# Performance work log

Measured on AMD Instinct MI355X. Metric: run time of the kernel, lower is better.

## Reference

```python
import jax, jax.numpy as jnp
import numpy as np

B, N, D, E, ET, L = 2, 50000, 64, 400000, 200000, 6
R_STRUCT = 4
EPS = 1e-5


def _ln(x, g, b):
    m = jnp.mean(x, axis=-1, keepdims=True)
    v = jnp.mean((x - m) ** 2, axis=-1, keepdims=True)
    return (x - m) * jax.lax.rsqrt(v + EPS) * g + b


def _nbf(boundary, src, dst, rel_e_fn, W, b, g, beta):
    # One RelNBFNet / TextRelNBFNet stack of GeneralizedRelationalConv layers:
    #   distmult message, sum aggregation with boundary self-loop message,
    #   linear([x, agg]) -> layernorm -> relu, short_cut residual.
    # boundary: [B, N, D]
    x = boundary
    for i in range(W.shape[0]):
        msg = x[:, src, :] * rel_e_fn(i)                    # [B, E, D]
        agg = jnp.zeros_like(x).at[:, dst, :].add(msg) + boundary
        h = jnp.concatenate([x, agg], axis=-1) @ W[i] + b[i]
        h = jax.nn.relu(_ln(h, g[i], beta[i]))
        x = h + x                                           # short_cut
    return x


def setup_inputs() -> dict:
    key = jax.random.key(0)
    ks = jax.random.split(key, 16)
    s = 0.05
    return {
        "rel_text_init": jax.random.normal(ks[0], (N, D), jnp.float32),
        "struct_rel": jax.random.normal(ks[1], (L, R_STRUCT, D), jnp.float32) * s,
        "struct_W": jax.random.normal(ks[2], (L, 2 * D, D), jnp.float32) * s,
        "struct_b": jnp.zeros((L, D), jnp.float32),
        "struct_g": jnp.ones((L, D), jnp.float32),
        "struct_beta": jnp.zeros((L, D), jnp.float32),
        "text_rel": jax.random.normal(ks[3], (L, 1, D), jnp.float32) * s,
        "text_W": jax.random.normal(ks[4], (L, 2 * D, D), jnp.float32) * s,
        "text_b": jnp.zeros((L, D), jnp.float32),
        "text_g": jnp.ones((L, D), jnp.float32),
        "text_beta": jnp.zeros((L, D), jnp.float32),
        "fuse_W1": jax.random.normal(ks[5], (2 * D, D), jnp.float32) * s,
        "fuse_b1": jnp.zeros((D,), jnp.float32),
        "fuse_W2": jax.random.normal(ks[6], (D, D), jnp.float32) * s,
        "fuse_b2": jnp.zeros((D,), jnp.float32),
        "h_index": jax.random.randint(ks[7], (B,), 0, N),
        "edge_index": jax.random.randint(ks[8], (2, E), 0, N),
        "edge_type": jax.random.randint(ks[9], (E,), 0, R_STRUCT),
        "text_edge_index": jax.random.randint(ks[10], (2, ET), 0, N),
    }


def reference(rel_text_init, struct_rel, struct_W, struct_b, struct_g, struct_beta,
              text_rel, text_W, text_b, text_g, text_beta,
              fuse_W1, fuse_b1, fuse_W2, fuse_b2,
              h_index, edge_index, edge_type, text_edge_index):
    # struct branch: boundary = indicator at query relation node
    boundary_s = jnp.zeros((B, N, D), rel_text_init.dtype).at[jnp.arange(B), h_index].add(1.0)
    h = _nbf(boundary_s, edge_index[0], edge_index[1],
             lambda i: struct_rel[i][edge_type],
             struct_W, struct_b, struct_g, struct_beta)
    # text branch: boundary = text-derived init features, single relation type
    boundary_t = jnp.broadcast_to(rel_text_init[None], (B, N, D))
    z = _nbf(boundary_t, text_edge_index[0], text_edge_index[1],
             lambda i: text_rel[i, 0][None, None, :],
             text_W, text_b, text_g, text_beta)
    # mlp fusion (alpha = 1.0)
    f = jax.nn.relu(jnp.concatenate([h, z], axis=-1) @ fuse_W1 + fuse_b1)
    return f @ fuse_W2 + fuse_b2
```

## Files before the change

### kernel.cpp

```cpp
#include <hip/hip_runtime.h>


__device__ __forceinline__ float bf2f(unsigned short u) {
    return __uint_as_float(((unsigned)u) << 16);
}
__device__ __forceinline__ unsigned short f2bf(float f) {
    unsigned u = __float_as_uint(f);
    u += 0x7FFF + ((u >> 16) & 1);
    return (unsigned short)(u >> 16);
}
#define PACK2(a, b) ((unsigned)f2bf(a) | ((unsigned)f2bf(b) << 16))

__device__ __forceinline__ float4 lnout(float4 A, float m, float inv,
                                        float4 xv, float4 gg, float4 bb) {
    float4 y;
    y.x = fmaxf((A.x - m) * inv * gg.x + bb.x, 0.f) + xv.x;
    y.y = fmaxf((A.y - m) * inv * gg.y + bb.y, 0.f) + xv.y;
    y.z = fmaxf((A.z - m) * inv * gg.z + bb.z, 0.f) + xv.z;
    y.w = fmaxf((A.w - m) * inv * gg.w + bb.w, 0.f) + xv.w;
    return y;
}

#define FMA4R(v, wbase, R0, R1, R2, R3) do {                                  \
    const float4* _w = (const float4*)(wbase); float4 _t;                     \
    _t=_w[0]; R0.x=fmaf(v,_t.x,R0.x); R0.y=fmaf(v,_t.y,R0.y); R0.z=fmaf(v,_t.z,R0.z); R0.w=fmaf(v,_t.w,R0.w); \
    _t=_w[1]; R1.x=fmaf(v,_t.x,R1.x); R1.y=fmaf(v,_t.y,R1.y); R1.z=fmaf(v,_t.z,R1.z); R1.w=fmaf(v,_t.w,R1.w); \
    _t=_w[2]; R2.x=fmaf(v,_t.x,R2.x); R2.y=fmaf(v,_t.y,R2.y); R2.z=fmaf(v,_t.z,R2.z); R2.w=fmaf(v,_t.w,R2.w); \
    _t=_w[3]; R3.x=fmaf(v,_t.x,R3.x); R3.y=fmaf(v,_t.y,R3.y); R3.z=fmaf(v,_t.z,R3.z); R3.w=fmaf(v,_t.w,R3.w); \
} while (0)

#define FMA4R2(v0, v1, wbase, P0,P1,P2,P3, Q0,Q1,Q2,Q3) do {                  \
    const float4* _w = (const float4*)(wbase); float4 _t;                     \
    _t=_w[0];                                                                 \
    P0.x=fmaf(v0,_t.x,P0.x); P0.y=fmaf(v0,_t.y,P0.y); P0.z=fmaf(v0,_t.z,P0.z); P0.w=fmaf(v0,_t.w,P0.w); \
    Q0.x=fmaf(v1,_t.x,Q0.x); Q0.y=fmaf(v1,_t.y,Q0.y); Q0.z=fmaf(v1,_t.z,Q0.z); Q0.w=fmaf(v1,_t.w,Q0.w); \
    _t=_w[1];                                                                 \
    P1.x=fmaf(v0,_t.x,P1.x); P1.y=fmaf(v0,_t.y,P1.y); P1.z=fmaf(v0,_t.z,P1.z); P1.w=fmaf(v0,_t.w,P1.w); \
    Q1.x=fmaf(v1,_t.x,Q1.x); Q1.y=fmaf(v1,_t.y,Q1.y); Q1.z=fmaf(v1,_t.z,Q1.z); Q1.w=fmaf(v1,_t.w,Q1.w); \
    _t=_w[2];                                                                 \
    P2.x=fmaf(v0,_t.x,P2.x); P2.y=fmaf(v0,_t.y,P2.y); P2.z=fmaf(v0,_t.z,P2.z); P2.w=fmaf(v0,_t.w,P2.w); \
    Q2.x=fmaf(v1,_t.x,Q2.x); Q2.y=fmaf(v1,_t.y,Q2.y); Q2.z=fmaf(v1,_t.z,Q2.z); Q2.w=fmaf(v1,_t.w,Q2.w); \
    _t=_w[3];                                                                 \
    P3.x=fmaf(v0,_t.x,P3.x); P3.y=fmaf(v0,_t.y,P3.y); P3.z=fmaf(v0,_t.z,P3.z); P3.w=fmaf(v0,_t.w,P3.w); \
    Q3.x=fmaf(v1,_t.x,Q3.x); Q3.y=fmaf(v1,_t.y,Q3.y); Q3.z=fmaf(v1,_t.z,Q3.z); Q3.w=fmaf(v1,_t.w,Q3.w); \
} while (0)

#define SUM4(Ai) ((Ai.x + Ai.y) + (Ai.z + Ai.w))
#define VAR4M(Ai, mm, vv) do { float _c;                                      \
    _c = Ai.x - mm; vv = fmaf(_c, _c, vv); _c = Ai.y - mm; vv = fmaf(_c, _c, vv); \
    _c = Ai.z - mm; vv = fmaf(_c, _c, vv); _c = Ai.w - mm; vv = fmaf(_c, _c, vv); \
} while (0)

#define RSEL(ty) (((ty) < 2) ? ((ty) == 0 ? r0 : r1) : ((ty) == 2 ? r2 : r3))

__global__ __launch_bounds__(256) void k_init_onehot(
    float* __restrict__ x, unsigned* __restrict__ xmir,
    const int* __restrict__ h_index, int N, int total, int b2)
{
    int idx = blockIdx.x * 256 + threadIdx.x;
    if (idx >= total) return;
    int row = idx >> 6;
    int b = row / N;
    int n = row - b * N;
    x[idx] = (n == h_index[b]) ? 1.0f : 0.0f;
    if (b2 && idx < N * 64) {
        int nn = idx >> 6;
        unsigned w = ((nn == h_index[0]) ? 0x3F80u : 0u)
                   | (((nn == h_index[1]) ? 0x3F80u : 0u) << 16);
        xmir[idx] = w;
    }
}

__global__ __launch_bounds__(256) void k_cast_init(
    const float* __restrict__ init, float* __restrict__ x,
    unsigned short* __restrict__ xbf, int total)
{
    int idx = blockIdx.x * 256 + threadIdx.x;
    if (idx >= total) return;
    float f = init[idx];
    x[idx] = f;
    xbf[idx] = f2bf(f);
}

__global__ __launch_bounds__(256) void k_hist_all(
    const int* __restrict__ dst_s, const int* __restrict__ dst_t,
    int* __restrict__ cnt_s, int* __restrict__ cnt_t, int E, int ET)
{
    int i = blockIdx.x * 256 + threadIdx.x;
    if (i < E) atomicAdd(&cnt_s[dst_s[i]], 1);
    else if (i < E + ET) atomicAdd(&cnt_t[dst_t[i - E]], 1);
}

__global__ __launch_bounds__(1024) void k_scan_blk2(
    const int* __restrict__ cnt_s, int* __restrict__ off_s, int* __restrict__ bsum_s,
    const int* __restrict__ cnt_t, int* __restrict__ off_t, int* __restrict__ bsum_t,
    int n, int nb)
{
    bool tpath = blockIdx.x >= nb;
    int lb = tpath ? blockIdx.x - nb : blockIdx.x;
    const int* cnt = tpath ? cnt_t : cnt_s;
    int* off = tpath ? off_t : off_s;
    int* bsum = tpath ? bsum_t : bsum_s;

    __shared__ int wsum[16], wpre[16], tot;
    int tid = threadIdx.x, lane = tid & 63, w = tid >> 6;
    int i = lb * 1024 + tid;
    int v = (i < n) ? cnt[i] : 0;
    int s = v;
    #pragma unroll
    for (int d = 1; d < 64; d <<= 1) {
        int t = __shfl_up(s, d);
        if (lane >= d) s += t;
    }
    if (lane == 63) wsum[w] = s;
    __syncthreads();
    if (w == 0 && lane < 16) {
        int ws = wsum[lane];
        int p = ws;
        #pragma unroll
        for (int d = 1; d < 16; d <<= 1) {
            int t = __shfl_up(p, d);
            if (lane >= d) p += t;
        }
        wpre[lane] = p - ws;
        if (lane == 15) tot = p;
    }
    __syncthreads();
    if (i < n) off[i + 1] = wpre[w] + s;
    if (tid == 0) {
        bsum[lb] = tot;
        if (lb == 0) off[0] = 0;
    }
}

__global__ __launch_bounds__(1024) void k_scan_top2(
    int* __restrict__ bsum_s, int* __restrict__ bsum_t, int nb)
{
    int* bsum = (blockIdx.x == 0) ? bsum_s : bsum_t;
    __shared__ int wsum[16], wpre[16];
    int tid = threadIdx.x, lane = tid & 63, w = tid >> 6;
    int v = (tid < nb) ? bsum[tid] : 0;
    int s = v;
    #pragma unroll
    for (int d = 1; d < 64; d <<= 1) {
        int t = __shfl_up(s, d);
        if (lane >= d) s += t;
    }
    if (lane == 63) wsum[w] = s;
    __syncthreads();
    if (w == 0 && lane < 16) {
        int ws = wsum[lane];
        int p = ws;
        #pragma unroll
        for (int d = 1; d < 16; d <<= 1) {
            int t = __shfl_up(p, d);
            if (lane >= d) p += t;
        }
        wpre[lane] = p - ws;
    }
    __syncthreads();
    if (tid < nb) bsum[tid] = wpre[w] + s - v;
}

__global__ __launch_bounds__(1024) void k_scan_add2(
    const int* __restrict__ bsum_s, int* __restrict__ off_s,
    const int* __restrict__ bsum_t, int* __restrict__ off_t, int n, int nb)
{
    bool tpath = blockIdx.x >= nb;
    int lb = tpath ? blockIdx.x - nb : blockIdx.x;
    int i = lb * 1024 + threadIdx.x;
    if (i < n) (tpath ? off_t : off_s)[i + 1] += (tpath ? bsum_t : bsum_s)[lb];
}

__global__ __launch_bounds__(256) void k_fill_all(
    const int* __restrict__ src_s, const int* __restrict__ dst_s,
    const int* __restrict__ etype,
    const int* __restrict__ off_s, int* __restrict__ cnt_s, int* __restrict__ pk_s,
    const int* __restrict__ src_t, const int* __restrict__ dst_t,
    const int* __restrict__ off_t, int* __restrict__ cnt_t, int* __restrict__ pk_t,
    int E, int ET)
{
    int i = blockIdx.x * 256 + threadIdx.x;
    if (i < E) {
        int d = dst_s[i];
        int pos = off_s[d] + atomicSub(&cnt_s[d], 1) - 1;
        pk_s[pos] = src_s[i] | (etype[i] << 27);
    } else if (i < E + ET) {
        int e = i - E;
        int d = dst_t[e];
        int pos = off_t[d] + atomicSub(&cnt_t[d], 1) - 1;
        pk_t[pos] = src_t[e];
    }
}

__global__ __launch_bounds__(256) void k_gather_all(
    const unsigned* __restrict__ xws, float* __restrict__ aggs,
    const int* __restrict__ offs, const int* __restrict__ pks,
    const float* __restrict__ rels,
    const int* __restrict__ hidx,
    const unsigned short* __restrict__ xbt, float* __restrict__ aggt,
    const int* __restrict__ offt, const int* __restrict__ pkt,
    const float* __restrict__ relt,
    const float* __restrict__ init,
    int N, int sblocks, int tblocks)
{
    int tid = threadIdx.x;
    int lane = tid & 63;
    bool isStruct; int lb;
    if (sblocks == tblocks) { isStruct = !(blockIdx.x & 1); lb = blockIdx.x >> 1; }
    else if ((int)blockIdx.x < sblocks) { isStruct = true; lb = blockIdx.x; }
    else { isStruct = false; lb = blockIdx.x - sblocks; }
    int n = (lb * 256 + tid) >> 6;
    if (n >= N) return;

    if (isStruct) {
        float r0 = rels[lane], r1 = rels[64 + lane];
        float r2 = rels[128 + lane], r3 = rels[192 + lane];
        float acc0 = (n == hidx[0]) ? 1.0f : 0.0f;
        float acc1 = (n == hidx[1]) ? 1.0f : 0.0f;
        int p0 = __builtin_amdgcn_readfirstlane(offs[n]);
        int p1 = __builtin_amdgcn_readfirstlane(offs[n + 1]);
        for (int p = p0; p < p1; p += 64) {
            int myPk = (p + lane < p1) ? pks[p + lane] : 0;
            int cnt = min(p1 - p, 64);
            int i = 0;
            for (; i + 8 <= cnt; i += 8) {
                int k0 = __shfl(myPk, i + 0), k1 = __shfl(myPk, i + 1);
                int k2 = __shfl(myPk, i + 2), k3 = __shfl(myPk, i + 3);
                int k4 = __shfl(myPk, i + 4), k5 = __shfl(myPk, i + 5);
                int k6 = __shfl(myPk, i + 6), k7 = __shfl(myPk, i + 7);
                unsigned w0 = xws[(size_t)(k0 & 0x03FFFFFF) * 64 + lane];
                unsigned w1 = xws[(size_t)(k1 & 0x03FFFFFF) * 64 + lane];
                unsigned w2 = xws[(size_t)(k2 & 0x03FFFFFF) * 64 + lane];
                unsigned w3 = xws[(size_t)(k3 & 0x03FFFFFF) * 64 + lane];
                unsigned w4 = xws[(size_t)(k4 & 0x03FFFFFF) * 64 + lane];
                unsigned w5 = xws[(size_t)(k5 & 0x03FFFFFF) * 64 + lane];
                unsigned w6 = xws[(size_t)(k6 & 0x03FFFFFF) * 64 + lane];
                unsigned w7 = xws[(size_t)(k7 & 0x03FFFFFF) * 64 + lane];
                int t0 = k0 >> 27, t1 = k1 >> 27, t2 = k2 >> 27, t3 = k3 >> 27;
                int t4 = k4 >> 27, t5 = k5 >> 27, t6 = k6 >> 27, t7 = k7 >> 27;
                float ra = RSEL(t0), rb = RSEL(t1), rc = RSEL(t2), rd = RSEL(t3);
                float re = RSEL(t4), rf = RSEL(t5), rg = RSEL(t6), rh = RSEL(t7);
                acc0 = fmaf(bf2f((unsigned short)w0), ra, acc0);
                acc1 = fmaf(bf2f((unsigned short)(w0 >> 16)), ra, acc1);
                acc0 = fmaf(bf2f((unsigned short)w1), rb, acc0);
                acc1 = fmaf(bf2f((unsigned short)(w1 >> 16)), rb, acc1);
                acc0 = fmaf(bf2f((unsigned short)w2), rc, acc0);
                acc1 = fmaf(bf2f((unsigned short)(w2 >> 16)), rc, acc1);
                acc0 = fmaf(bf2f((unsigned short)w3), rd, acc0);
                acc1 = fmaf(bf2f((unsigned short)(w3 >> 16)), rd, acc1);
                acc0 = fmaf(bf2f((unsigned short)w4), re, acc0);
                acc1 = fmaf(bf2f((unsigned short)(w4 >> 16)), re, acc1);
                acc0 = fmaf(bf2f((unsigned short)w5), rf, acc0);
                acc1 = fmaf(bf2f((unsigned short)(w5 >> 16)), rf, acc1);
                acc0 = fmaf(bf2f((unsigned short)w6), rg, acc0);
                acc1 = fmaf(bf2f((unsigned short)(w6 >> 16)), rg, acc1);
                acc0 = fmaf(bf2f((unsigned short)w7), rh, acc0);
                acc1 = fmaf(bf2f((unsigned short)(w7 >> 16)), rh, acc1);
            }
            for (; i < cnt; ++i) {
                int pk = __shfl(myPk, i);
                int s = pk & 0x03FFFFFF, ty = pk >> 27;
                float r = RSEL(ty);
                unsigned w = xws[(size_t)s * 64 + lane];
                acc0 = fmaf(bf2f((unsigned short)w), r, acc0);
                acc1 = fmaf(bf2f((unsigned short)(w >> 16)), r, acc1);
            }
        }
        aggs[(size_t)n * 64 + lane] = acc0;
        aggs[(size_t)(N + n) * 64 + lane] = acc1;
    } else {
        float r = relt[lane];
        float acc = init[(size_t)n * 64 + lane];
        float acc2 = 0.f;
        int p0 = __builtin_amdgcn_readfirstlane(offt[n]);
        int p1 = __builtin_amdgcn_readfirstlane(offt[n + 1]);
        for (int p = p0; p < p1; p += 64) {
            int myPk = (p + lane < p1) ? pkt[p + lane] : 0;
            int cnt = min(p1 - p, 64);
            int i = 0;
            for (; i + 8 <= cnt; i += 8) {
                int s0 = __shfl(myPk, i + 0), s1 = __shfl(myPk, i + 1);
                int s2 = __shfl(myPk, i + 2), s3 = __shfl(myPk, i + 3);
                int s4 = __shfl(myPk, i + 4), s5 = __shfl(myPk, i + 5);
                int s6 = __shfl(myPk, i + 6), s7 = __shfl(myPk, i + 7);
                float a = bf2f(xbt[(size_t)s0 * 64 + lane]), b = bf2f(xbt[(size_t)s1 * 64 + lane]);
                float c = bf2f(xbt[(size_t)s2 * 64 + lane]), d = bf2f(xbt[(size_t)s3 * 64 + lane]);
                float e = bf2f(xbt[(size_t)s4 * 64 + lane]), f = bf2f(xbt[(size_t)s5 * 64 + lane]);
                float g = bf2f(xbt[(size_t)s6 * 64 + lane]), h = bf2f(xbt[(size_t)s7 * 64 + lane]);
                acc = fmaf(a, r, acc);  acc2 = fmaf(b, r, acc2);
                acc = fmaf(c, r, acc);  acc2 = fmaf(d, r, acc2);
                acc = fmaf(e, r, acc);  acc2 = fmaf(f, r, acc2);
                acc = fmaf(g, r, acc);  acc2 = fmaf(h, r, acc2);
            }
            for (; i < cnt; ++i) {
                int s = __shfl(myPk, i);
                acc = fmaf(bf2f(xbt[(size_t)s * 64 + lane]), r, acc);
            }
        }
        aggt[(size_t)n * 64 + lane] = acc + acc2;
    }
}

__global__ __launch_bounds__(256) void k_gather_struct_gen(
    const float* __restrict__ x, float* __restrict__ agg,
    const int* __restrict__ off, const int* __restrict__ packed,
    const float* __restrict__ rel, const int* __restrict__ h_index,
    int N, int BN)
{
    int wid = (blockIdx.x * 256 + threadIdx.x) >> 6;
    int lane = threadIdx.x & 63;
    if (wid >= BN) return;
    int b = wid / N;
    int n = wid - b * N;
    float r0 = rel[lane], r1 = rel[64 + lane];
    float r2 = rel[128 + lane], r3 = rel[192 + lane];
    const float* xb = x + (size_t)b * N * 64;
    float acc = (n == h_index[b]) ? 1.0f : 0.0f;
    int p0 = off[n], p1 = off[n + 1];
    for (int p = p0; p < p1; ++p) {
        int pk = packed[p];
        int s = pk & 0x03FFFFFF, ty = pk >> 27;
        acc = fmaf(xb[(size_t)s * 64 + lane], RSEL(ty), acc);
    }
    agg[(size_t)wid * 64 + lane] = acc;
}

__global__ __launch_bounds__(256) void k_update_all(
    const float* __restrict__ Ws, const float* __restrict__ bs_,
    const float* __restrict__ gs, const float* __restrict__ betas,
    float* __restrict__ xs, unsigned short* __restrict__ mirs,
    const float* __restrict__ aggs, int rows_s,
    const float* __restrict__ Wt, const float* __restrict__ bt_,
    const float* __restrict__ gt_, const float* __restrict__ betat,
    float* __restrict__ xt, unsigned short* __restrict__ mirt,
    const float* __restrict__ aggt, int rows_t,
    int bs_blocks, int bt_blocks, int Nn, int b2)
{
    bool tpath; int lb;
    if (bs_blocks == 2 * bt_blocks) {
        int m3 = blockIdx.x % 3, d3 = blockIdx.x / 3;
        if (m3 != 2) { tpath = false; lb = d3 * 2 + m3; }
        else { tpath = true; lb = d3; }
    } else if ((int)blockIdx.x < bs_blocks) { tpath = false; lb = blockIdx.x; }
    else { tpath = true; lb = blockIdx.x - bs_blocks; }

    const float* W    = tpath ? Wt : Ws;
    const float* bias = tpath ? bt_ : bs_;
    const float* g    = tpath ? gt_ : gs;
    const float* beta = tpath ? betat : betas;
    float* x          = tpath ? xt : xs;
    const float* agg  = tpath ? aggt : aggs;
    int rows          = tpath ? rows_t : rows_s;

    __shared__ float Wl[128 * 64];
    __shared__ float bl[64], gl[64], bel[64];
    int tid = threadIdx.x;
    {
        const float4* W4 = (const float4*)W;
        float4* Wl4 = (float4*)Wl;
        #pragma unroll
        for (int i = 0; i < 8; ++i) Wl4[tid + i * 256] = W4[tid + i * 256];
        if (tid < 64) { bl[tid] = bias[tid]; gl[tid] = g[tid]; bel[tid] = beta[tid]; }
    }
    __syncthreads();

    int gt2 = lb * 256 + tid;
    int pair = gt2 >> 2;
    int q = gt2 & 3, jc = q * 16;

    int r0i, r1i;
    bool h1;
    if (!tpath && b2) {
        if (pair >= Nn) return;
        r0i = pair; r1i = Nn + pair; h1 = true;
    } else {
        r0i = pair * 2; r1i = r0i + 1;
        if (r0i >= rows) return;
        h1 = (r1i < rows);
    }
    const float* xr0 = x + (size_t)r0i * 64;
    const float* ar0 = agg + (size_t)r0i * 64;
    const float* xr1 = h1 ? x + (size_t)r1i * 64 : xr0;
    const float* ar1 = h1 ? agg + (size_t)r1i * 64 : ar0;

    const float4* bj = (const float4*)(bl + jc);
    float4 A0 = bj[0], A1 = bj[1], A2 = bj[2], A3 = bj[3];
    float4 B0 = bj[0], B1 = bj[1], B2 = bj[2], B3 = bj[3];

    #pragma unroll
    for (int kb = 0; kb < 64; kb += 4) {
        float4 i0 = *(const float4*)(xr0 + kb);
        float4 i1 = *(const float4*)(xr1 + kb);
        FMA4R2(i0.x, i1.x, Wl + (kb + 0) * 64 + jc, A0,A1,A2,A3, B0,B1,B2,B3);
        FMA4R2(i0.y, i1.y, Wl + (kb + 1) * 64 + jc, A0,A1,A2,A3, B0,B1,B2,B3);
        FMA4R2(i0.z, i1.z, Wl + (kb + 2) * 64 + jc, A0,A1,A2,A3, B0,B1,B2,B3);
        FMA4R2(i0.w, i1.w, Wl + (kb + 3) * 64 + jc, A0,A1,A2,A3, B0,B1,B2,B3);
    }
    #pragma unroll
    for (int kb = 0; kb < 64; kb += 4) {
        float4 i0 = *(const float4*)(ar0 + kb);
        float4 i1 = *(const float4*)(ar1 + kb);
        FMA4R2(i0.x, i1.x, Wl + (64 + kb + 0) * 64 + jc, A0,A1,A2,A3, B0,B1,B2,B3);
        FMA4R2(i0.y, i1.y, Wl + (64 + kb + 1) * 64 + jc, A0,A1,A2,A3, B0,B1,B2,B3);
        FMA4R2(i0.z, i1.z, Wl + (64 + kb + 2) * 64 + jc, A0,A1,A2,A3, B0,B1,B2,B3);
        FMA4R2(i0.w, i1.w, Wl + (64 + kb + 3) * 64 + jc, A0,A1,A2,A3, B0,B1,B2,B3);
    }

    float ls0 = SUM4(A0) + SUM4(A1) + SUM4(A2) + SUM4(A3);
    float ls1 = SUM4(B0) + SUM4(B1) + SUM4(B2) + SUM4(B3);
    ls0 += __shfl_xor(ls0, 1); ls0 += __shfl_xor(ls0, 2);
    ls1 += __shfl_xor(ls1, 1); ls1 += __shfl_xor(ls1, 2);
    float m0 = ls0 * (1.0f / 64.0f), m1 = ls1 * (1.0f / 64.0f);
    float v0 = 0.f, v1 = 0.f;
    VAR4M(A0, m0, v0); VAR4M(A1, m0, v0); VAR4M(A2, m0, v0); VAR4M(A3, m0, v0);
    VAR4M(B0, m1, v1); VAR4M(B1, m1, v1); VAR4M(B2, m1, v1); VAR4M(B3, m1, v1);
    v0 += __shfl_xor(v0, 1); v0 += __shfl_xor(v0, 2);
    v1 += __shfl_xor(v1, 1); v1 += __shfl_xor(v1, 2);
    float inv0 = rsqrtf(v0 * (1.0f / 64.0f) + 1e-5f);
    float inv1 = rsqrtf(v1 * (1.0f / 64.0f) + 1e-5f);

    const float4* gg4 = (const float4*)(gl + jc);
    const float4* bb4 = (const float4*)(bel + jc);

    float4 ya0 = lnout(A0, m0, inv0, ((const float4*)(xr0 + jc))[0], gg4[0], bb4[0]);
    float4 ya1 = lnout(A1, m0, inv0, ((const float4*)(xr0 + jc))[1], gg4[1], bb4[1]);
    float4 ya2 = lnout(A2, m0, inv0, ((const float4*)(xr0 + jc))[2], gg4[2], bb4[2]);
    float4 ya3 = lnout(A3, m0, inv0, ((const float4*)(xr0 + jc))[3], gg4[3], bb4[3]);
    {
        float4* xw0 = (float4*)(x + (size_t)r0i * 64 + jc);
        xw0[0] = ya0; xw0[1] = ya1; xw0[2] = ya2; xw0[3] = ya3;
    }
    if (h1) {
        float4 yb0 = lnout(B0, m1, inv1, ((const float4*)(xr1 + jc))[0], gg4[0], bb4[0]);
        float4 yb1 = lnout(B1, m1, inv1, ((const float4*)(xr1 + jc))[1], gg4[1], bb4[1]);
        float4 yb2 = lnout(B2, m1, inv1, ((const float4*)(xr1 + jc))[2], gg4[2], bb4[2]);
        float4 yb3 = lnout(B3, m1, inv1, ((const float4*)(xr1 + jc))[3], gg4[3], bb4[3]);
        float4* xw1 = (float4*)(x + (size_t)r1i * 64 + jc);
        xw1[0] = yb0; xw1[1] = yb1; xw1[2] = yb2; xw1[3] = yb3;

        if (tpath) {
            uint2* mt = (uint2*)(mirt + (size_t)r0i * 64 + jc);
            mt[0] = make_uint2(PACK2(ya0.x, ya0.y), PACK2(ya0.z, ya0.w));
            mt[1] = make_uint2(PACK2(ya1.x, ya1.y), PACK2(ya1.z, ya1.w));
            mt[2] = make_uint2(PACK2(ya2.x, ya2.y), PACK2(ya2.z, ya2.w));
            mt[3] = make_uint2(PACK2(ya3.x, ya3.y), PACK2(ya3.z, ya3.w));
            uint2* mt1 = (uint2*)(mirt + (size_t)r1i * 64 + jc);
            mt1[0] = make_uint2(PACK2(yb0.x, yb0.y), PACK2(yb0.z, yb0.w));
            mt1[1] = make_uint2(PACK2(yb1.x, yb1.y), PACK2(yb1.z, yb1.w));
            mt1[2] = make_uint2(PACK2(yb2.x, yb2.y), PACK2(yb2.z, yb2.w));
            mt1[3] = make_uint2(PACK2(yb3.x, yb3.y), PACK2(yb3.z, yb3.w));
        } else if (b2) {
            uint4* mw = (uint4*)((unsigned*)mirs + (size_t)r0i * 64 + jc);
            mw[0] = make_uint4(PACK2(ya0.x, yb0.x), PACK2(ya0.y, yb0.y),
                               PACK2(ya0.z, yb0.z), PACK2(ya0.w, yb0.w));
            mw[1] = make_uint4(PACK2(ya1.x, yb1.x), PACK2(ya1.y, yb1.y),
                               PACK2(ya1.z, yb1.z), PACK2(ya1.w, yb1.w));
            mw[2] = make_uint4(PACK2(ya2.x, yb2.x), PACK2(ya2.y, yb2.y),
                               PACK2(ya2.z, yb2.z), PACK2(ya2.w, yb2.w));
            mw[3] = make_uint4(PACK2(ya3.x, yb3.x), PACK2(ya3.y, yb3.y),
                               PACK2(ya3.z, yb3.z), PACK2(ya3.w, yb3.w));
        }
    } else if (tpath) {
        uint2* mt = (uint2*)(mirt + (size_t)r0i * 64 + jc);
        mt[0] = make_uint2(PACK2(ya0.x, ya0.y), PACK2(ya0.z, ya0.w));
        mt[1] = make_uint2(PACK2(ya1.x, ya1.y), PACK2(ya1.z, ya1.w));
        mt[2] = make_uint2(PACK2(ya2.x, ya2.y), PACK2(ya2.z, ya2.w));
        mt[3] = make_uint2(PACK2(ya3.x, ya3.y), PACK2(ya3.z, ya3.w));
    }
}

__global__ __launch_bounds__(256) void k_fuse(
    const float* __restrict__ W1, const float* __restrict__ b1,
    const float* __restrict__ W2, const float* __restrict__ b2,
    float* __restrict__ out, const float* __restrict__ z, int N, int rows)
{
    __shared__ float W1l[128 * 64];
    __shared__ float W2l[64 * 64];
    __shared__ float b1l[64], b2l[64];
    int tid = threadIdx.x;
    {
        const float4* Wa = (const float4*)W1;
        float4* Wla = (float4*)W1l;
        #pragma unroll
        for (int i = 0; i < 8; ++i) Wla[tid + i * 256] = Wa[tid + i * 256];
        const float4* Wb = (const float4*)W2;
        float4* Wlb = (float4*)W2l;
        #pragma unroll
        for (int i = 0; i < 4; ++i) Wlb[tid + i * 256] = Wb[tid + i * 256];
        if (tid < 64) { b1l[tid] = b1[tid]; b2l[tid] = b2[tid]; }
    }
    __syncthreads();

    int gt2 = blockIdx.x * 256 + tid;
    int row = gt2 >> 2;
    int q = gt2 & 3;
    int jc = q * 16;
    if (row >= rows) return;
    int n = row % N;
    const float* hr = out + (size_t)row * 64;
    const float* zr = z + (size_t)n * 64;
    int lane = tid & 63;

    const float4* bj = (const float4*)(b1l + jc);
    float4 F0 = bj[0], F1 = bj[1], F2 = bj[2], F3 = bj[3];
    #pragma unroll
    for (int kb = 0; kb < 64; kb += 4) {
        float4 iv = *(const float4*)(hr + kb);
        FMA4R(iv.x, W1l + (kb + 0) * 64 + jc, F0, F1, F2, F3);
        FMA4R(iv.y, W1l + (kb + 1) * 64 + jc, F0, F1, F2, F3);
        FMA4R(iv.z, W1l + (kb + 2) * 64 + jc, F0, F1, F2, F3);
        FMA4R(iv.w, W1l + (kb + 3) * 64 + jc, F0, F1, F2, F3);
    }
    #pragma unroll
    for (int kb = 0; kb < 64; kb += 4) {
        float4 iv = *(const float4*)(zr + kb);
        FMA4R(iv.x, W1l + (64 + kb + 0) * 64 + jc, F0, F1, F2, F3);
        FMA4R(iv.y, W1l + (64 + kb + 1) * 64 + jc, F0, F1, F2, F3);
        FMA4R(iv.z, W1l + (64 + kb + 2) * 64 + jc, F0, F1, F2, F3);
        FMA4R(iv.w, W1l + (64 + kb + 3) * 64 + jc, F0, F1, F2, F3);
    }
    F0.x = fmaxf(F0.x, 0.f); F0.y = fmaxf(F0.y, 0.f); F0.z = fmaxf(F0.z, 0.f); F0.w = fmaxf(F0.w, 0.f);
    F1.x = fmaxf(F1.x, 0.f); F1.y = fmaxf(F1.y, 0.f); F1.z = fmaxf(F1.z, 0.f); F1.w = fmaxf(F1.w, 0.f);
    F2.x = fmaxf(F2.x, 0.f); F2.y = fmaxf(F2.y, 0.f); F2.z = fmaxf(F2.z, 0.f); F2.w = fmaxf(F2.w, 0.f);
    F3.x = fmaxf(F3.x, 0.f); F3.y = fmaxf(F3.y, 0.f); F3.z = fmaxf(F3.z, 0.f); F3.w = fmaxf(F3.w, 0.f);

    const float4* bj2 = (const float4*)(b2l + jc);
    float4 O0 = bj2[0], O1 = bj2[1], O2 = bj2[2], O3 = bj2[3];
    int srcLane = (lane & ~3) | ((q + 1) & 3);
    #pragma unroll
    for (int s = 0; s < 4; ++s) {
        int c = (q + s) & 3;
        const float* w2 = W2l + (c * 16) * 64 + jc;
        FMA4R(F0.x, w2 + 0 * 64,  O0, O1, O2, O3);
        FMA4R(F0.y, w2 + 1 * 64,  O0, O1, O2, O3);
        FMA4R(F0.z, w2 + 2 * 64,  O0, O1, O2, O3);
        FMA4R(F0.w, w2 + 3 * 64,  O0, O1, O2, O3);
        FMA4R(F1.x, w2 + 4 * 64,  O0, O1, O2, O3);
        FMA4R(F1.y, w2 + 5 * 64,  O0, O1, O2, O3);
        FMA4R(F1.z, w2 + 6 * 64,  O0, O1, O2, O3);
        FMA4R(F1.w, w2 + 7 * 64,  O0, O1, O2, O3);
        FMA4R(F2.x, w2 + 8 * 64,  O0, O1, O2, O3);
        FMA4R(F2.y, w2 + 9 * 64,  O0, O1, O2, O3);
        FMA4R(F2.z, w2 + 10 * 64, O0, O1, O2, O3);
        FMA4R(F2.w, w2 + 11 * 64, O0, O1, O2, O3);
        FMA4R(F3.x, w2 + 12 * 64, O0, O1, O2, O3);
        FMA4R(F3.y, w2 + 13 * 64, O0, O1, O2, O3);
        FMA4R(F3.z, w2 + 14 * 64, O0, O1, O2, O3);
        FMA4R(F3.w, w2 + 15 * 64, O0, O1, O2, O3);
        if (s < 3) {
            F0.x = __shfl(F0.x, srcLane); F0.y = __shfl(F0.y, srcLane);
            F0.z = __shfl(F0.z, srcLane); F0.w = __shfl(F0.w, srcLane);
            F1.x = __shfl(F1.x, srcLane); F1.y = __shfl(F1.y, srcLane);
            F1.z = __shfl(F1.z, srcLane); F1.w = __shfl(F1.w, srcLane);
            F2.x = __shfl(F2.x, srcLane); F2.y = __shfl(F2.y, srcLane);
            F2.z = __shfl(F2.z, srcLane); F2.w = __shfl(F2.w, srcLane);
            F3.x = __shfl(F3.x, srcLane); F3.y = __shfl(F3.y, srcLane);
            F3.z = __shfl(F3.z, srcLane); F3.w = __shfl(F3.w, srcLane);
        }
    }
    float4* ow4 = (float4*)(out + (size_t)row * 64 + jc);
    ow4[0] = O0; ow4[1] = O1; ow4[2] = O2; ow4[3] = O3;
}

extern "C" void kernel_launch(void* const* d_in, const int* in_sizes, int n_in,
                              void* d_out, int out_size, void* d_ws, size_t ws_size,
                              hipStream_t stream)
{
    const float* rel_text_init = (const float*)d_in[0];
    const float* struct_rel    = (const float*)d_in[1];
    const float* struct_W      = (const float*)d_in[2];
    const float* struct_b      = (const float*)d_in[3];
    const float* struct_g      = (const float*)d_in[4];
    const float* struct_beta   = (const float*)d_in[5];
    const float* text_rel      = (const float*)d_in[6];
    const float* text_W        = (const float*)d_in[7];
    const float* text_b        = (const float*)d_in[8];
    const float* text_g        = (const float*)d_in[9];
    const float* text_beta     = (const float*)d_in[10];
    const float* fuse_W1       = (const float*)d_in[11];
    const float* fuse_b1       = (const float*)d_in[12];
    const float* fuse_W2       = (const float*)d_in[13];
    const float* fuse_b2       = (const float*)d_in[14];
    const int*   h_index       = (const int*)d_in[15];
    const int*   edge_index    = (const int*)d_in[16];
    const int*   edge_type     = (const int*)d_in[17];
    const int*   text_edge_idx = (const int*)d_in[18];

    const int B  = in_sizes[15];
    const int N  = in_sizes[0] / 64;
    const int E  = in_sizes[17];
    const int ET = in_sizes[18] / 2;
    const int L  = in_sizes[3] / 64;
    const int R  = in_sizes[1] / (L * 64);

    const int* src  = edge_index;
    const int* dst  = edge_index + E;
    const int* tsrc = text_edge_idx;
    const int* tdst = text_edge_idx + ET;

    float* x_t   = (float*)d_ws;
    float* agg_t = x_t + (size_t)N * 64;
    float* agg_s = agg_t + (size_t)N * 64;
    unsigned short* xbf_s = (unsigned short*)(agg_s + (size_t)B * N * 64);
    unsigned short* xbf_t = xbf_s + (size_t)B * N * 64;
    int*   cnt_s = (int*)(xbf_t + (size_t)N * 64);
    int*   off_s = cnt_s + N;
    int*   pk_s  = off_s + N + 1;
    int*   cnt_t = pk_s + E;
    int*   off_t = cnt_t + N;
    int*   pk_t  = off_t + N + 1;
    int*   bsum_s = pk_t + ET;
    int*   bsum_t = bsum_s + 1024;

    float* x_s = (float*)d_out;

    const size_t nd  = (size_t)N * 64;
    const int rows_s = B * N;
    const int tot_s  = rows_s * 64;
    const int nb     = (N + 1023) / 1024;
    const int b2     = (B == 2) ? 1 : 0;

    const int gb_init   = (tot_s + 255) / 256;
    const int gb_castt  = ((int)nd + 255) / 256;
    const int gb_hist   = (E + ET + 255) / 256;
    const int gb_wave_n = (N * 64 + 255) / 256;
    const int pairs_s   = b2 ? N : (rows_s + 1) / 2;
    const int pairs_t   = (N + 1) / 2;
    const int bs_blocks = (pairs_s * 4 + 255) / 256;
    const int bt_blocks = (pairs_t * 4 + 255) / 256;
    const int gb_fuse   = (rows_s * 4 + 255) / 256;

    hipMemsetAsync(cnt_s, 0, (size_t)N * 4, stream);
    hipMemsetAsync(cnt_t, 0, (size_t)N * 4, stream);
    k_hist_all<<<gb_hist, 256, 0, stream>>>(dst, tdst, cnt_s, cnt_t, E, ET);
    k_scan_blk2<<<2 * nb, 1024, 0, stream>>>(cnt_s, off_s, bsum_s,
                                             cnt_t, off_t, bsum_t, N, nb);
    k_scan_top2<<<2, 1024, 0, stream>>>(bsum_s, bsum_t, nb);
    k_scan_add2<<<2 * nb, 1024, 0, stream>>>(bsum_s, off_s, bsum_t, off_t, N, nb);
    k_fill_all<<<gb_hist, 256, 0, stream>>>(src, dst, edge_type, off_s, cnt_s, pk_s,
                                            tsrc, tdst, off_t, cnt_t, pk_t, E, ET);

    k_init_onehot<<<gb_init, 256, 0, stream>>>(
        x_s, (unsigned*)xbf_s, h_index, N, tot_s, b2);
    k_cast_init<<<gb_castt, 256, 0, stream>>>(rel_text_init, x_t, xbf_t, (int)nd);

    for (int i = 0; i < L; ++i) {
        if (b2) {
            k_gather_all<<<2 * gb_wave_n, 256, 0, stream>>>(
                (const unsigned*)xbf_s, agg_s, off_s, pk_s,
                struct_rel + (size_t)i * R * 64, h_index,
                xbf_t, agg_t, off_t, pk_t, text_rel + (size_t)i * 64, rel_text_init,
                N, gb_wave_n, gb_wave_n);
        } else {
            k_gather_struct_gen<<<(rows_s * 64 + 255) / 256, 256, 0, stream>>>(
                x_s, agg_s, off_s, pk_s,
                struct_rel + (size_t)i * R * 64, h_index, N, rows_s);
            k_gather_all<<<gb_wave_n, 256, 0, stream>>>(
                (const unsigned*)xbf_s, agg_s, off_s, pk_s,
                struct_rel + (size_t)i * R * 64, h_index,
                xbf_t, agg_t, off_t, pk_t, text_rel + (size_t)i * 64, rel_text_init,
                N, 0, gb_wave_n);
        }
        k_update_all<<<bs_blocks + bt_blocks, 256, 0, stream>>>(
            struct_W + (size_t)i * 128 * 64, struct_b + i * 64,
            struct_g + i * 64, struct_beta + i * 64, x_s, xbf_s, agg_s, rows_s,
            text_W + (size_t)i * 128 * 64, text_b + i * 64,
            text_g + i * 64, text_beta + i * 64, x_t, xbf_t, agg_t, N,
            bs_blocks, bt_blocks, N, b2);
    }

    k_fuse<<<gb_fuse, 256, 0, stream>>>(
        fuse_W1, fuse_b1, fuse_W2, fuse_b2, x_s, x_t, N, rows_s);
}
```

Measured before the change: 725.9 us.

## Fuse per-layer gather and linear/layernorm update into one kernel with ping-pong mirrors

Merges the separate gather and update kernels into one per-layer kernel. Each block gathers 64 nodes into a swizzled LDS tile, loads W into LDS, then runs the linear, layernorm, relu and residual in place. The bf16 mirrors are double-buffered across layers so a block can write new features while other blocks still read the old ones. This removes the agg round-trip through global memory and one launch per layer. In exchange it uses 64KB of LDS per block, which limits occupancy for the latency-bound gather.

Result: slower. 1.922 ms (+164.8%).

```diff
diff --git a/kernel.cpp b/kernel.cpp
--- a/kernel.cpp
+++ b/kernel.cpp
@@ -10,6 +10,7 @@
     return (unsigned short)(u >> 16);
 }
 #define PACK2(a, b) ((unsigned)f2bf(a) | ((unsigned)f2bf(b) << 16))
+#define SWZ(r) (((r) & 7) << 2)
 
 __device__ __forceinline__ float4 lnout(float4 A, float m, float inv,
                                         float4 xv, float4 gg, float4 bb) {
@@ -193,112 +194,262 @@
     }
 }
 
-__global__ __launch_bounds__(256) void k_gather_all(
-    const unsigned* __restrict__ xws, float* __restrict__ aggs,
+__global__ __launch_bounds__(256) void k_layer_all(
+    const unsigned* __restrict__ mi_s, unsigned* __restrict__ mo_s,
+    float* __restrict__ xs,
     const int* __restrict__ offs, const int* __restrict__ pks,
-    const float* __restrict__ rels,
-    const int* __restrict__ hidx,
-    const unsigned short* __restrict__ xbt, float* __restrict__ aggt,
+    const float* __restrict__ rels, const int* __restrict__ hidx,
+    const float* __restrict__ Ws, const float* __restrict__ bs_,
+    const float* __restrict__ gs, const float* __restrict__ betas,
+    const unsigned short* __restrict__ mi_t, unsigned short* __restrict__ mo_t,
+    float* __restrict__ xt,
     const int* __restrict__ offt, const int* __restrict__ pkt,
-    const float* __restrict__ relt,
-    const float* __restrict__ init,
+    const float* __restrict__ relt, const float* __restrict__ tinit,
+    const float* __restrict__ Wt, const float* __restrict__ bt_,
+    const float* __restrict__ gt_, const float* __restrict__ betat,
     int N, int sblocks, int tblocks)
 {
-    int tid = threadIdx.x;
-    int lane = tid & 63;
+    __shared__ float Wl[128 * 64];
+    __shared__ float accL[128 * 64];
+    __shared__ float bl[64], gl[64], bel[64];
+
+    int tid = threadIdx.x, lane = tid & 63, w = tid >> 6;
     bool isStruct; int lb;
     if (sblocks == tblocks) { isStruct = !(blockIdx.x & 1); lb = blockIdx.x >> 1; }
     else if ((int)blockIdx.x < sblocks) { isStruct = true; lb = blockIdx.x; }
     else { isStruct = false; lb = blockIdx.x - sblocks; }
-    int n = (lb * 256 + tid) >> 6;
-    if (n >= N) return;
+
+    {
+        const float* W = isStruct ? Ws : Wt;
+        const float4* W4 = (const float4*)W;
+        float4* Wl4 = (float4*)Wl;
+        #pragma unroll
+        for (int i = 0; i < 8; ++i) Wl4[tid + i * 256] = W4[tid + i * 256];
+        if (tid < 64) {
+            bl[tid]  = (isStruct ? bs_ : bt_)[tid];
+            gl[tid]  = (isStruct ? gs : gt_)[tid];
+            bel[tid] = (isStruct ? betas : betat)[tid];
+        }
+    }
+    int nodeBase = lb * 64;
 
     if (isStruct) {
         float r0 = rels[lane], r1 = rels[64 + lane];
         float r2 = rels[128 + lane], r3 = rels[192 + lane];
-        float acc0 = (n == hidx[0]) ? 1.0f : 0.0f;
-        float acc1 = (n == hidx[1]) ? 1.0f : 0.0f;
-        int p0 = __builtin_amdgcn_readfirstlane(offs[n]);
-        int p1 = __builtin_amdgcn_readfirstlane(offs[n + 1]);
-        for (int p = p0; p < p1; p += 64) {
-            int myPk = (p + lane < p1) ? pks[p + lane] : 0;
-            int cnt = min(p1 - p, 64);
-            int i = 0;
-            for (; i + 8 <= cnt; i += 8) {
-                int k0 = __shfl(myPk, i + 0), k1 = __shfl(myPk, i + 1);
-                int k2 = __shfl(myPk, i + 2), k3 = __shfl(myPk, i + 3);
-                int k4 = __shfl(myPk, i + 4), k5 = __shfl(myPk, i + 5);
-                int k6 = __shfl(myPk, i + 6), k7 = __shfl(myPk, i + 7);
-                unsigned w0 = xws[(size_t)(k0 & 0x03FFFFFF) * 64 + lane];
-                unsigned w1 = xws[(size_t)(k1 & 0x03FFFFFF) * 64 + lane];
-                unsigned w2 = xws[(size_t)(k2 & 0x03FFFFFF) * 64 + lane];
-                unsigned w3 = xws[(size_t)(k3 & 0x03FFFFFF) * 64 + lane];
-                unsigned w4 = xws[(size_t)(k4 & 0x03FFFFFF) * 64 + lane];
-                unsigned w5 = xws[(size_t)(k5 & 0x03FFFFFF) * 64 + lane];
-                unsigned w6 = xws[(size_t)(k6 & 0x03FFFFFF) * 64 + lane];
-                unsigned w7 = xws[(size_t)(k7 & 0x03FFFFFF) * 64 + lane];
-                int t0 = k0 >> 27, t1 = k1 >> 27, t2 = k2 >> 27, t3 = k3 >> 27;
-                int t4 = k4 >> 27, t5 = k5 >> 27, t6 = k6 >> 27, t7 = k7 >> 27;
-                float ra = RSEL(t0), rb = RSEL(t1), rc = RSEL(t2), rd = RSEL(t3);
-                float re = RSEL(t4), rf = RSEL(t5), rg = RSEL(t6), rh = RSEL(t7);
-                acc0 = fmaf(bf2f((unsigned short)w0), ra, acc0);
-                acc1 = fmaf(bf2f((unsigned short)(w0 >> 16)), ra, acc1);
-                acc0 = fmaf(bf2f((unsigned short)w1), rb, acc0);
-                acc1 = fmaf(bf2f((unsigned short)(w1 >> 16)), rb, acc1);
-                acc0 = fmaf(bf2f((unsigned short)w2), rc, acc0);
-                acc1 = fmaf(bf2f((unsigned short)(w2 >> 16)), rc, acc1);
-                acc0 = fmaf(bf2f((unsigned short)w3), rd, acc0);
-                acc1 = fmaf(bf2f((unsigned short)(w3 >> 16)), rd, acc1);
-                acc0 = fmaf(bf2f((unsigned short)w4), re, acc0);
-                acc1 = fmaf(bf2f((unsigned short)(w4 >> 16)), re, acc1);
-                acc0 = fmaf(bf2f((unsigned short)w5), rf, acc0);
-                acc1 = fmaf(bf2f((unsigned short)(w5 >> 16)), rf, acc1);
-                acc0 = fmaf(bf2f((unsigned short)w6), rg, acc0);
-                acc1 = fmaf(bf2f((unsigned short)(w6 >> 16)), rg, acc1);
-                acc0 = fmaf(bf2f((unsigned short)w7), rh, acc0);
-                acc1 = fmaf(bf2f((unsigned short)(w7 >> 16)), rh, acc1);
+        int h0 = hidx[0], h1i = hidx[1];
+        for (int j = 0; j < 16; ++j) {
+            int n = nodeBase + w * 16 + j;
+            if (n >= N) break;
+            float acc0 = (n == h0) ? 1.0f : 0.0f;
+            float acc1 = (n == h1i) ? 1.0f : 0.0f;
+            int p0 = __builtin_amdgcn_readfirstlane(offs[n]);
+            int p1 = __builtin_amdgcn_readfirstlane(offs[n + 1]);
+            for (int p = p0; p < p1; p += 64) {
+                int myPk = (p + lane < p1) ? pks[p + lane] : 0;
+                int cnt = min(p1 - p, 64);
+                int i = 0;
+                for (; i + 8 <= cnt; i += 8) {
+                    int k0 = __shfl(myPk, i + 0), k1 = __shfl(myPk, i + 1);
+                    int k2 = __shfl(myPk, i + 2), k3 = __shfl(myPk, i + 3);
+                    int k4 = __shfl(myPk, i + 4), k5 = __shfl(myPk, i + 5);
+                    int k6 = __shfl(myPk, i + 6), k7 = __shfl(myPk, i + 7);
+                    unsigned w0 = mi_s[(size_t)(k0 & 0x03FFFFFF) * 64 + lane];
+                    unsigned w1 = mi_s[(size_t)(k1 & 0x03FFFFFF) * 64 + lane];
+                    unsigned w2 = mi_s[(size_t)(k2 & 0x03FFFFFF) * 64 + lane];
+                    unsigned w3 = mi_s[(size_t)(k3 & 0x03FFFFFF) * 64 + lane];
+                    unsigned w4 = mi_s[(size_t)(k4 & 0x03FFFFFF) * 64 + lane];
+                    unsigned w5 = mi_s[(size_t)(k5 & 0x03FFFFFF) * 64 + lane];
+                    unsigned w6 = mi_s[(size_t)(k6 & 0x03FFFFFF) * 64 + lane];
+                    unsigned w7 = mi_s[(size_t)(k7 & 0x03FFFFFF) * 64 + lane];
+                    int t0 = k0 >> 27, t1 = k1 >> 27, t2 = k2 >> 27, t3 = k3 >> 27;
+                    int t4 = k4 >> 27, t5 = k5 >> 27, t6 = k6 >> 27, t7 = k7 >> 27;
+                    float ra = RSEL(t0), rb = RSEL(t1), rc = RSEL(t2), rd = RSEL(t3);
+                    float re = RSEL(t4), rf = RSEL(t5), rg = RSEL(t6), rh = RSEL(t7);
+                    acc0 = fmaf(bf2f((unsigned short)w0), ra, acc0);
+                    acc1 = fmaf(bf2f((unsigned short)(w0 >> 16)), ra, acc1);
+                    acc0 = fmaf(bf2f((unsigned short)w1), rb, acc0);
+                    acc1 = fmaf(bf2f((unsigned short)(w1 >> 16)), rb, acc1);
+                    acc0 = fmaf(bf2f((unsigned short)w2), rc, acc0);
+                    acc1 = fmaf(bf2f((unsigned short)(w2 >> 16)), rc, acc1);
+                    acc0 = fmaf(bf2f((unsigned short)w3), rd, acc0);
+                    acc1 = fmaf(bf2f((unsigned short)(w3 >> 16)), rd, acc1);
+                    acc0 = fmaf(bf2f((unsigned short)w4), re, acc0);
+                    acc1 = fmaf(bf2f((unsigned short)(w4 >> 16)), re, acc1);
+                    acc0 = fmaf(bf2f((unsigned short)w5), rf, acc0);
+                    acc1 = fmaf(bf2f((unsigned short)(w5 >> 16)), rf, acc1);
+                    acc0 = fmaf(bf2f((unsigned short)w6), rg, acc0);
+                    acc1 = fmaf(bf2f((unsigned short)(w6 >> 16)), rg, acc1);
+                    acc0 = fmaf(bf2f((unsigned short)w7), rh, acc0);
+                    acc1 = fmaf(bf2f((unsigned short)(w7 >> 16)), rh, acc1);
+                }
+                for (; i < cnt; ++i) {
+                    int pk = __shfl(myPk, i);
+                    int s = pk & 0x03FFFFFF, ty = pk >> 27;
+                    float r = RSEL(ty);
+                    unsigned ww = mi_s[(size_t)s * 64 + lane];
+                    acc0 = fmaf(bf2f((unsigned short)ww), r, acc0);
+                    acc1 = fmaf(bf2f((unsigned short)(ww >> 16)), r, acc1);
+                }
             }
-            for (; i < cnt; ++i) {
-                int pk = __shfl(myPk, i);
-                int s = pk & 0x03FFFFFF, ty = pk >> 27;
-                float r = RSEL(ty);
-                unsigned w = xws[(size_t)s * 64 + lane];
-                acc0 = fmaf(bf2f((unsigned short)w), r, acc0);
-                acc1 = fmaf(bf2f((unsigned short)(w >> 16)), r, acc1);
-            }
-        }
-        aggs[(size_t)n * 64 + lane] = acc0;
-        aggs[(size_t)(N + n) * 64 + lane] = acc1;
+            int r0loc = w * 16 + j, r1loc = 64 + r0loc;
+            accL[r0loc * 64 + (lane ^ SWZ(r0loc))] = acc0;
+            accL[r1loc * 64 + (lane ^ SWZ(r1loc))] = acc1;
+        }
+        __syncthreads();
+
+        int pair = tid >> 2, q = tid & 3, jc = q * 16;
+        int n = nodeBase + pair;
+        if (n >= N) return;
+        const float* xr0 = xs + (size_t)n * 64;
+        const float* xr1 = xs + ((size_t)N + n) * 64;
+        const float* aL0 = accL + pair * 64;
+        const float* aL1 = accL + (64 + pair) * 64;
+        int swz = SWZ(pair);
+
+        const float4* bj = (const float4*)(bl + jc);
+        float4 A0 = bj[0], A1 = bj[1], A2 = bj[2], A3 = bj[3];
+        float4 B0 = bj[0], B1 = bj[1], B2 = bj[2], B3 = bj[3];
+
+        #pragma unroll
+        for (int kb = 0; kb < 64; kb += 4) {
+            float4 i0 = *(const float4*)(xr0 + kb);
+            float4 i1 = *(const float4*)(xr1 + kb);
+            FMA4R2(i0.x, i1.x, Wl + (kb + 0) * 64 + jc, A0,A1,A2,A3, B0,B1,B2,B3);
+            FMA4R2(i0.y, i1.y, Wl + (kb + 1) * 64 + jc, A0,A1,A2,A3, B0,B1,B2,B3);
+            FMA4R2(i0.z, i1.z, Wl + (kb + 2) * 64 + jc, A0,A1,A2,A3, B0,B1,B2,B3);
+            FMA4R2(i0.w, i1.w, Wl + (kb + 3) * 64 + jc, A0,A1,A2,A3, B0,B1,B2,B3);
+        }
+        #pragma unroll
+        for (int kb = 0; kb < 64; kb += 4) {
+            float4 i0 = *(const float4*)(aL0 + (kb ^ swz));
+            float4 i1 = *(const float4*)(aL1 + (kb ^ swz));
+            FMA4R2(i0.x, i1.x, Wl + (64 + kb + 0) * 64 + jc, A0,A1,A2,A3, B0,B1,B2,B3);
+            FMA4R2(i0.y, i1.y, Wl + (64 + kb + 1) * 64 + jc, A0,A1,A2,A3, B0,B1,B2,B3);
+            FMA4R2(i0.z, i1.z, Wl + (64 + kb + 2) * 64 + jc, A0,A1,A2,A3, B0,B1,B2,B3);
+            FMA4R2(i0.w, i1.w, Wl + (64 + kb + 3) * 64 + jc, A0,A1,A2,A3, B0,B1,B2,B3);
+        }
+
+        float ls0 = SUM4(A0) + SUM4(A1) + SUM4(A2) + SUM4(A3);
+        float ls1 = SUM4(B0) + SUM4(B1) + SUM4(B2) + SUM4(B3);
+        ls0 += __shfl_xor(ls0, 1); ls0 += __shfl_xor(ls0, 2);
+        ls1 += __shfl_xor(ls1, 1); ls1 += __shfl_xor(ls1, 2);
+        float m0 = ls0 * (1.0f / 64.0f), m1 = ls1 * (1.0f / 64.0f);
+        float v0 = 0.f, v1 = 0.f;
+        VAR4M(A0, m0, v0); VAR4M(A1, m0, v0); VAR4M(A2, m0, v0); VAR4M(A3, m0, v0);
+        VAR4M(B0, m1, v1); VAR4M(B1, m1, v1); VAR4M(B2, m1, v1); VAR4M(B3, m1, v1);
+        v0 += __shfl_xor(v0, 1); v0 += __shfl_xor(v0, 2);
+        v1 += __shfl_xor(v1, 1); v1 += __shfl_xor(v1, 2);
+        float inv0 = rsqrtf(v0 * (1.0f / 64.0f) + 1e-5f);
+        float inv1 = rsqrtf(v1 * (1.0f / 64.0f) + 1e-5f);
+
+        const float4* gg4 = (const float4*)(gl + jc);
+        const float4* bb4 = (const float4*)(bel + jc);
+        float4 ya0 = lnout(A0, m0, inv0, ((const float4*)(xr0 + jc))[0], gg4[0], bb4[0]);
+        float4 ya1 = lnout(A1, m0, inv0, ((const float4*)(xr0 + jc))[1], gg4[1], bb4[1]);
+        float4 ya2 = lnout(A2, m0, inv0, ((const float4*)(xr0 + jc))[2], gg4[2], bb4[2]);
+        float4 ya3 = lnout(A3, m0, inv0, ((const float4*)(xr0 + jc))[3], gg4[3], bb4[3]);
+        float4 yb0 = lnout(B0, m1, inv1, ((const float4*)(xr1 + jc))[0], gg4[0], bb4[0]);
+        float4 yb1 = lnout(B1, m1, inv1, ((const float4*)(xr1 + jc))[1], gg4[1], bb4[1]);
+        float4 yb2 = lnout(B2, m1, inv1, ((const float4*)(xr1 + jc))[2], gg4[2], bb4[2]);
+        float4 yb3 = lnout(B3, m1, inv1, ((const float4*)(xr1 + jc))[3], gg4[3], bb4[3]);
+
+        float4* xw0 = (float4*)(xs + (size_t)n * 64 + jc);
+        xw0[0] = ya0; xw0[1] = ya1; xw0[2] = ya2; xw0[3] = ya3;
+        float4* xw1 = (float4*)(xs + ((size_t)N + n) * 64 + jc);
+        xw1[0] = yb0; xw1[1] = yb1; xw1[2] = yb2; xw1[3] = yb3;
+
+        uint4* mw = (uint4*)(mo_s + (size_t)n * 64 + jc);
+        mw[0] = make_uint4(PACK2(ya0.x, yb0.x), PACK2(ya0.y, yb0.y),
+                           PACK2(ya0.z, yb0.z), PACK2(ya0.w, yb0.w));
+        mw[1] = make_uint4(PACK2(ya1.x, yb1.x), PACK2(ya1.y, yb1.y),
+                           PACK2(ya1.z, yb1.z), PACK2(ya1.w, yb1.w));
+        mw[2] = make_uint4(PACK2(ya2.x, yb2.x), PACK2(ya2.y, yb2.y),
+                           PACK2(ya2.z, yb2.z), PACK2(ya2.w, yb2.w));
+        mw[3] = make_uint4(PACK2(ya3.x, yb3.x), PACK2(ya3.y, yb3.y),
+                           PACK2(ya3.z, yb3.z), PACK2(ya3.w, yb3.w));
     } else {
         float r = relt[lane];
-        float acc = init[(size_t)n * 64 + lane];
-        float acc2 = 0.f;
-        int p0 = __builtin_amdgcn_readfirstlane(offt[n]);
-        int p1 = __builtin_amdgcn_readfirstlane(offt[n + 1]);
-        for (int p = p0; p < p1; p += 64) {
-            int myPk = (p + lane < p1) ? pkt[p + lane] : 0;
-            int cnt = min(p1 - p, 64);
-            int i = 0;
-            for (; i + 8 <= cnt; i += 8) {
-                int s0 = __shfl(myPk, i + 0), s1 = __shfl(myPk, i + 1);
-                int s2 = __shfl(myPk, i + 2), s3 = __shfl(myPk, i + 3);
-                int s4 = __shfl(myPk, i + 4), s5 = __shfl(myPk, i + 5);
-                int s6 = __shfl(myPk, i + 6), s7 = __shfl(myPk, i + 7);
-                float a = bf2f(xbt[(size_t)s0 * 64 + lane]), b = bf2f(xbt[(size_t)s1 * 64 + lane]);
-                float c = bf2f(xbt[(size_t)s2 * 64 + lane]), d = bf2f(xbt[(size_t)s3 * 64 + lane]);
-                float e = bf2f(xbt[(size_t)s4 * 64 + lane]), f = bf2f(xbt[(size_t)s5 * 64 + lane]);
-                float g = bf2f(xbt[(size_t)s6 * 64 + lane]), h = bf2f(xbt[(size_t)s7 * 64 + lane]);
-                acc = fmaf(a, r, acc);  acc2 = fmaf(b, r, acc2);
-                acc = fmaf(c, r, acc);  acc2 = fmaf(d, r, acc2);
-                acc = fmaf(e, r, acc);  acc2 = fmaf(f, r, acc2);
-                acc = fmaf(g, r, acc);  acc2 = fmaf(h, r, acc2);
+        for (int j = 0; j < 16; ++j) {
+            int n = nodeBase + w * 16 + j;
+            if (n >= N) break;
+            float acc = tinit[(size_t)n * 64 + lane];
+            float acc2 = 0.f;
+            int p0 = __builtin_amdgcn_readfirstlane(offt[n]);
+            int p1 = __builtin_amdgcn_readfirstlane(offt[n + 1]);
+            for (int p = p0; p < p1; p += 64) {
+                int myPk = (p + lane < p1) ? pkt[p + lane] : 0;
+                int cnt = min(p1 - p, 64);
+                int i = 0;
+                for (; i + 8 <= cnt; i += 8) {
+                    int s0 = __shfl(myPk, i + 0), s1 = __shfl(myPk, i + 1);
+                    int s2 = __shfl(myPk, i + 2), s3 = __shfl(myPk, i + 3);
+                    int s4 = __shfl(myPk, i + 4), s5 = __shfl(myPk, i + 5);
+                    int s6 = __shfl(myPk, i + 6), s7 = __shfl(myPk, i + 7);
+                    float a = bf2f(mi_t[(size_t)s0 * 64 + lane]), b = bf2f(mi_t[(size_t)s1 * 64 + lane]);
+                    float c = bf2f(mi_t[(size_t)s2 * 64 + lane]), d = bf2f(mi_t[(size_t)s3 * 64 + lane]);
+                    float e = bf2f(mi_t[(size_t)s4 * 64 + lane]), f = bf2f(mi_t[(size_t)s5 * 64 + lane]);
+                    float g = bf2f(mi_t[(size_t)s6 * 64 + lane]), h = bf2f(mi_t[(size_t)s7 * 64 + lane]);
+                    acc = fmaf(a, r, acc);  acc2 = fmaf(b, r, acc2);
+                    acc = fmaf(c, r, acc);  acc2 = fmaf(d, r, acc2);
+                    acc = fmaf(e, r, acc);  acc2 = fmaf(f, r, acc2);
+                    acc = fmaf(g, r, acc);  acc2 = fmaf(h, r, acc2);
+                }
+                for (; i < cnt; ++i) {
+                    int s = __shfl(myPk, i);
+                    acc = fmaf(bf2f(mi_t[(size_t)s * 64 + lane]), r, acc);
+                }
             }
-            for (; i < cnt; ++i) {
-                int s = __shfl(myPk, i);
-                acc = fmaf(bf2f(xbt[(size_t)s * 64 + lane]), r, acc);
-            }
-        }
-        aggt[(size_t)n * 64 + lane] = acc + acc2;
+            int rl = w * 16 + j;
+            accL[rl * 64 + (lane ^ SWZ(rl))] = acc + acc2;
+        }
+        __syncthreads();
+
+        int pair = tid >> 2, q = tid & 3, jc = q * 16;
+        int n = nodeBase + pair;
+        if (n >= N) return;
+        const float* xr = xt + (size_t)n * 64;
+        const float* aL = accL + pair * 64;
+        int swz = SWZ(pair);
+
+        const float4* bj = (const float4*)(bl + jc);
+        float4 A0 = bj[0], A1 = bj[1], A2 = bj[2], A3 = bj[3];
+        #pragma unroll
+        for (int kb = 0; kb < 64; kb += 4) {
+            float4 iv = *(const float4*)(xr + kb);
+            FMA4R(iv.x, Wl + (kb + 0) * 64 + jc, A0, A1, A2, A3);
+            FMA4R(iv.y, Wl + (kb + 1) * 64 + jc, A0, A1, A2, A3);
+            FMA4R(iv.z, Wl + (kb + 2) * 64 + jc, A0, A1, A2, A3);
+            FMA4R(iv.w, Wl + (kb + 3) * 64 + jc, A0, A1, A2, A3);
+        }
+        #pragma unroll
+        for (int kb = 0; kb < 64; kb += 4) {
+            float4 iv = *(const float4*)(aL + (kb ^ swz));
+            FMA4R(iv.x, Wl + (64 + kb + 0) * 64 + jc, A0, A1, A2, A3);
+            FMA4R(iv.y, Wl + (64 + kb + 1) * 64 + jc, A0, A1, A2, A3);
+            FMA4R(iv.z, Wl + (64 + kb + 2) * 64 + jc, A0, A1, A2, A3);
+            FMA4R(iv.w, Wl + (64 + kb + 3) * 64 + jc, A0, A1, A2, A3);
+        }
+        float ls = SUM4(A0) + SUM4(A1) + SUM4(A2) + SUM4(A3);
+        ls += __shfl_xor(ls, 1); ls += __shfl_xor(ls, 2);
+        float m = ls * (1.0f / 64.0f);
+        float vs = 0.f;
+        VAR4M(A0, m, vs); VAR4M(A1, m, vs); VAR4M(A2, m, vs); VAR4M(A3, m, vs);
+        vs += __shfl_xor(vs, 1); vs += __shfl_xor(vs, 2);
+        float inv = rsqrtf(vs * (1.0f / 64.0f) + 1e-5f);
+
+        const float4* gg4 = (const float4*)(gl + jc);
+        const float4* bb4 = (const float4*)(bel + jc);
+        float4 y0 = lnout(A0, m, inv, ((const float4*)(xr + jc))[0], gg4[0], bb4[0]);
+        float4 y1 = lnout(A1, m, inv, ((const float4*)(xr + jc))[1], gg4[1], bb4[1]);
+        float4 y2 = lnout(A2, m, inv, ((const float4*)(xr + jc))[2], gg4[2], bb4[2]);
+        float4 y3 = lnout(A3, m, inv, ((const float4*)(xr + jc))[3], gg4[3], bb4[3]);
+        float4* xw = (float4*)(xt + (size_t)n * 64 + jc);
+        xw[0] = y0; xw[1] = y1; xw[2] = y2; xw[3] = y3;
+        uint2* mt = (uint2*)(mo_t + (size_t)n * 64 + jc);
+        mt[0] = make_uint2(PACK2(y0.x, y0.y), PACK2(y0.z, y0.w));
+        mt[1] = make_uint2(PACK2(y1.x, y1.y), PACK2(y1.z, y1.w));
+        mt[2] = make_uint2(PACK2(y2.x, y2.y), PACK2(y2.z, y2.w));
+        mt[3] = make_uint2(PACK2(y3.x, y3.y), PACK2(y3.z, y3.w));
     }
 }
 
@@ -326,33 +477,11 @@
     agg[(size_t)wid * 64 + lane] = acc;
 }
 
-__global__ __launch_bounds__(256) void k_update_all(
-    const float* __restrict__ Ws, const float* __restrict__ bs_,
-    const float* __restrict__ gs, const float* __restrict__ betas,
-    float* __restrict__ xs, unsigned short* __restrict__ mirs,
-    const float* __restrict__ aggs, int rows_s,
-    const float* __restrict__ Wt, const float* __restrict__ bt_,
-    const float* __restrict__ gt_, const float* __restrict__ betat,
-    float* __restrict__ xt, unsigned short* __restrict__ mirt,
-    const float* __restrict__ aggt, int rows_t,
-    int bs_blocks, int bt_blocks, int Nn, int b2)
-{
-    bool tpath; int lb;
-    if (bs_blocks == 2 * bt_blocks) {
-        int m3 = blockIdx.x % 3, d3 = blockIdx.x / 3;
-        if (m3 != 2) { tpath = false; lb = d3 * 2 + m3; }
-        else { tpath = true; lb = d3; }
-    } else if ((int)blockIdx.x < bs_blocks) { tpath = false; lb = blockIdx.x; }
-    else { tpath = true; lb = blockIdx.x - bs_blocks; }
-
-    const float* W    = tpath ? Wt : Ws;
-    const float* bias = tpath ? bt_ : bs_;
-    const float* g    = tpath ? gt_ : gs;
-    const float* beta = tpath ? betat : betas;
-    float* x          = tpath ? xt : xs;
-    const float* agg  = tpath ? aggt : aggs;
-    int rows          = tpath ? rows_t : rows_s;
-
+__global__ __launch_bounds__(256) void k_update_gen(
+    const float* __restrict__ W, const float* __restrict__ bias,
+    const float* __restrict__ g, const float* __restrict__ beta,
+    float* __restrict__ x, const float* __restrict__ agg, int rows)
+{
     __shared__ float Wl[128 * 64];
     __shared__ float bl[64], gl[64], bel[64];
     int tid = threadIdx.x;
@@ -364,110 +493,44 @@
         if (tid < 64) { bl[tid] = bias[tid]; gl[tid] = g[tid]; bel[tid] = beta[tid]; }
     }
     __syncthreads();
-
-    int gt2 = lb * 256 + tid;
-    int pair = gt2 >> 2;
-    int q = gt2 & 3, jc = q * 16;
-
-    int r0i, r1i;
-    bool h1;
-    if (!tpath && b2) {
-        if (pair >= Nn) return;
-        r0i = pair; r1i = Nn + pair; h1 = true;
-    } else {
-        r0i = pair * 2; r1i = r0i + 1;
-        if (r0i >= rows) return;
-        h1 = (r1i < rows);
-    }
-    const float* xr0 = x + (size_t)r0i * 64;
-    const float* ar0 = agg + (size_t)r0i * 64;
-    const float* xr1 = h1 ? x + (size_t)r1i * 64 : xr0;
-    const float* ar1 = h1 ? agg + (size_t)r1i * 64 : ar0;
-
+    int gt2 = blockIdx.x * 256 + tid;
+    int row = gt2 >> 2, q = gt2 & 3, jc = q * 16;
+    if (row >= rows) return;
+    const float* xr = x + (size_t)row * 64;
+    const float* ar = agg + (size_t)row * 64;
     const float4* bj = (const float4*)(bl + jc);
     float4 A0 = bj[0], A1 = bj[1], A2 = bj[2], A3 = bj[3];
-    float4 B0 = bj[0], B1 = bj[1], B2 = bj[2], B3 = bj[3];
-
     #pragma unroll
     for (int kb = 0; kb < 64; kb += 4) {
-        float4 i0 = *(const float4*)(xr0 + kb);
-        float4 i1 = *(const float4*)(xr1 + kb);
-        FMA4R2(i0.x, i1.x, Wl + (kb + 0) * 64 + jc, A0,A1,A2,A3, B0,B1,B2,B3);
-        FMA4R2(i0.y, i1.y, Wl + (kb + 1) * 64 + jc, A0,A1,A2,A3, B0,B1,B2,B3);
-        FMA4R2(i0.z, i1.z, Wl + (kb + 2) * 64 + jc, A0,A1,A2,A3, B0,B1,B2,B3);
-        FMA4R2(i0.w, i1.w, Wl + (kb + 3) * 64 + jc, A0,A1,A2,A3, B0,B1,B2,B3);
+        float4 iv = *(const float4*)(xr + kb);
+        FMA4R(iv.x, Wl + (kb + 0) * 64 + jc, A0, A1, A2, A3);
+        FMA4R(iv.y, Wl + (kb + 1) * 64 + jc, A0, A1, A2, A3);
+        FMA4R(iv.z, Wl + (kb + 2) * 64 + jc, A0, A1, A2, A3);
+        FMA4R(iv.w, Wl + (kb + 3) * 64 + jc, A0, A1, A2, A3);
     }
     #pragma unroll
     for (int kb = 0; kb < 64; kb += 4) {
-        float4 i0 = *(const float4*)(ar0 + kb);
-        float4 i1 = *(const float4*)(ar1 + kb);
-        FMA4R2(i0.x, i1.x, Wl + (64 + kb + 0) * 64 + jc, A0,A1,A2,A3, B0,B1,B2,B3);
-        FMA4R2(i0.y, i1.y, Wl + (64 + kb + 1) * 64 + jc, A0,A1,A2,A3, B0,B1,B2,B3);
-        FMA4R2(i0.z, i1.z, Wl + (64 + kb + 2) * 64 + jc, A0,A1,A2,A3, B0,B1,B2,B3);
-        FMA4R2(i0.w, i1.w, Wl + (64 + kb + 3) * 64 + jc, A0,A1,A2,A3, B0,B1,B2,B3);
-    }
-
-    float ls0 = SUM4(A0) + SUM4(A1) + SUM4(A2) + SUM4(A3);
-    float ls1 = SUM4(B0) + SUM4(B1) + SUM4(B2) + SUM4(B3);
-    ls0 += __shfl_xor(ls0, 1); ls0 += __shfl_xor(ls0, 2);
-    ls1 += __shfl_xor(ls1, 1); ls1 += __shfl_xor(ls1, 2);
-    float m0 = ls0 * (1.0f / 64.0f), m1 = ls1 * (1.0f / 64.0f);
-    float v0 = 0.f, v1 = 0.f;
-    VAR4M(A0, m0, v0); VAR4M(A1, m0, v0); VAR4M(A2, m0, v0); VAR4M(A3, m0, v0);
-    VAR4M(B0, m1, v1); VAR4M(B1, m1, v1); VAR4M(B2, m1, v1); VAR4M(B3, m1, v1);
-    v0 += __shfl_xor(v0, 1); v0 += __shfl_xor(v0, 2);
-    v1 += __shfl_xor(v1, 1); v1 += __shfl_xor(v1, 2);
-    float inv0 = rsqrtf(v0 * (1.0f / 64.0f) + 1e-5f);
-    float inv1 = rsqrtf(v1 * (1.0f / 64.0f) + 1e-5f);
-
+        float4 iv = *(const float4*)(ar + kb);
+        FMA4R(iv.x, Wl + (64 + kb + 0) * 64 + jc, A0, A1, A2, A3);
+        FMA4R(iv.y, Wl + (64 + kb + 1) * 64 + jc, A0, A1, A2, A3);
+        FMA4R(iv.z, Wl + (64 + kb + 2) * 64 + jc, A0, A1, A2, A3);
+        FMA4R(iv.w, Wl + (64 + kb + 3) * 64 + jc, A0, A1, A2, A3);
+    }
+    float ls = SUM4(A0) + SUM4(A1) + SUM4(A2) + SUM4(A3);
+    ls += __shfl_xor(ls, 1); ls += __shfl_xor(ls, 2);
+    float m = ls * (1.0f / 64.0f);
+    float vs = 0.f;
+    VAR4M(A0, m, vs); VAR4M(A1, m, vs); VAR4M(A2, m, vs); VAR4M(A3, m, vs);
+    vs += __shfl_xor(vs, 1); vs += __shfl_xor(vs, 2);
+    float inv = rsqrtf(vs * (1.0f / 64.0f) + 1e-5f);
     const float4* gg4 = (const float4*)(gl + jc);
     const float4* bb4 = (const float4*)(bel + jc);
-
-    float4 ya0 = lnout(A0, m0, inv0, ((const float4*)(xr0 + jc))[0], gg4[0], bb4[0]);
-    float4 ya1 = lnout(A1, m0, inv0, ((const float4*)(xr0 + jc))[1], gg4[1], bb4[1]);
-    float4 ya2 = lnout(A2, m0, inv0, ((const float4*)(xr0 + jc))[2], gg4[2], bb4[2]);
-    float4 ya3 = lnout(A3, m0, inv0, ((const float4*)(xr0 + jc))[3], gg4[3], bb4[3]);
-    {
-        float4* xw0 = (float4*)(x + (size_t)r0i * 64 + jc);
-        xw0[0] = ya0; xw0[1] = ya1; xw0[2] = ya2; xw0[3] = ya3;
-    }
-    if (h1) {
-        float4 yb0 = lnout(B0, m1, inv1, ((const float4*)(xr1 + jc))[0], gg4[0], bb4[0]);
-        float4 yb1 = lnout(B1, m1, inv1, ((const float4*)(xr1 + jc))[1], gg4[1], bb4[1]);
-        float4 yb2 = lnout(B2, m1, inv1, ((const float4*)(xr1 + jc))[2], gg4[2], bb4[2]);
-        float4 yb3 = lnout(B3, m1, inv1, ((const float4*)(xr1 + jc))[3], gg4[3], bb4[3]);
-        float4* xw1 = (float4*)(x + (size_t)r1i * 64 + jc);
-        xw1[0] = yb0; xw1[1] = yb1; xw1[2] = yb2; xw1[3] = yb3;
-
-        if (tpath) {
-            uint2* mt = (uint2*)(mirt + (size_t)r0i * 64 + jc);
-            mt[0] = make_uint2(PACK2(ya0.x, ya0.y), PACK2(ya0.z, ya0.w));
-            mt[1] = make_uint2(PACK2(ya1.x, ya1.y), PACK2(ya1.z, ya1.w));
-            mt[2] = make_uint2(PACK2(ya2.x, ya2.y), PACK2(ya2.z, ya2.w));
-            mt[3] = make_uint2(PACK2(ya3.x, ya3.y), PACK2(ya3.z, ya3.w));
-            uint2* mt1 = (uint2*)(mirt + (size_t)r1i * 64 + jc);
-            mt1[0] = make_uint2(PACK2(yb0.x, yb0.y), PACK2(yb0.z, yb0.w));
-            mt1[1] = make_uint2(PACK2(yb1.x, yb1.y), PACK2(yb1.z, yb1.w));
-            mt1[2] = make_uint2(PACK2(yb2.x, yb2.y), PACK2(yb2.z, yb2.w));
-            mt1[3] = make_uint2(PACK2(yb3.x, yb3.y), PACK2(yb3.z, yb3.w));
-        } else if (b2) {
-            uint4* mw = (uint4*)((unsigned*)mirs + (size_t)r0i * 64 + jc);
-            mw[0] = make_uint4(PACK2(ya0.x, yb0.x), PACK2(ya0.y, yb0.y),
-                               PACK2(ya0.z, yb0.z), PACK2(ya0.w, yb0.w));
-            mw[1] = make_uint4(PACK2(ya1.x, yb1.x), PACK2(ya1.y, yb1.y),
-                               PACK2(ya1.z, yb1.z), PACK2(ya1.w, yb1.w));
-            mw[2] = make_uint4(PACK2(ya2.x, yb2.x), PACK2(ya2.y, yb2.y),
-                               PACK2(ya2.z, yb2.z), PACK2(ya2.w, yb2.w));
-            mw[3] = make_uint4(PACK2(ya3.x, yb3.x), PACK2(ya3.y, yb3.y),
-                               PACK2(ya3.z, yb3.z), PACK2(ya3.w, yb3.w));
-        }
-    } else if (tpath) {
-        uint2* mt = (uint2*)(mirt + (size_t)r0i * 64 + jc);
-        mt[0] = make_uint2(PACK2(ya0.x, ya0.y), PACK2(ya0.z, ya0.w));
-        mt[1] = make_uint2(PACK2(ya1.x, ya1.y), PACK2(ya1.z, ya1.w));
-        mt[2] = make_uint2(PACK2(ya2.x, ya2.y), PACK2(ya2.z, ya2.w));
-        mt[3] = make_uint2(PACK2(ya3.x, ya3.y), PACK2(ya3.z, ya3.w));
-    }
+    float4 y0 = lnout(A0, m, inv, ((const float4*)(xr + jc))[0], gg4[0], bb4[0]);
+    float4 y1 = lnout(A1, m, inv, ((const float4*)(xr + jc))[1], gg4[1], bb4[1]);
+    float4 y2 = lnout(A2, m, inv, ((const float4*)(xr + jc))[2], gg4[2], bb4[2]);
+    float4 y3 = lnout(A3, m, inv, ((const float4*)(xr + jc))[3], gg4[3], bb4[3]);
+    float4* xw = (float4*)(x + (size_t)row * 64 + jc);
+    xw[0] = y0; xw[1] = y1; xw[2] = y2; xw[3] = y3;
 }
 
 __global__ __launch_bounds__(256) void k_fuse(
@@ -599,19 +662,20 @@
     const int* tsrc = text_edge_idx;
     const int* tdst = text_edge_idx + ET;
 
-    float* x_t   = (float*)d_ws;
-    float* agg_t = x_t + (size_t)N * 64;
-    float* agg_s = agg_t + (size_t)N * 64;
-    unsigned short* xbf_s = (unsigned short*)(agg_s + (size_t)B * N * 64);
-    unsigned short* xbf_t = xbf_s + (size_t)B * N * 64;
-    int*   cnt_s = (int*)(xbf_t + (size_t)N * 64);
-    int*   off_s = cnt_s + N;
-    int*   pk_s  = off_s + N + 1;
-    int*   cnt_t = pk_s + E;
-    int*   off_t = cnt_t + N;
-    int*   pk_t  = off_t + N + 1;
-    int*   bsum_s = pk_t + ET;
-    int*   bsum_t = bsum_s + 1024;
+    float* x_t = (float*)d_ws;
+    unsigned* mirA_s = (unsigned*)(x_t + (size_t)N * 64);
+    unsigned* mirB_s = mirA_s + (size_t)N * 64;
+    unsigned short* mirA_t = (unsigned short*)(mirB_s + (size_t)N * 64);
+    unsigned short* mirB_t = mirA_t + (size_t)N * 64;
+    int* cnt_s = (int*)(mirB_t + (size_t)N * 64);
+    int* off_s = cnt_s + N;
+    int* pk_s  = off_s + N + 1;
+    int* cnt_t = pk_s + E;
+    int* off_t = cnt_t + N;
+    int* pk_t  = off_t + N + 1;
+    int* bsum_s = pk_t + ET;
+    int* bsum_t = bsum_s + 1024;
+    float* agg_gen = (float*)mirA_s;
 
     float* x_s = (float*)d_out;
 
@@ -620,16 +684,11 @@
     const int tot_s  = rows_s * 64;
     const int nb     = (N + 1023) / 1024;
     const int b2     = (B == 2) ? 1 : 0;
-
-    const int gb_init   = (tot_s + 255) / 256;
-    const int gb_castt  = ((int)nd + 255) / 256;
-    const int gb_hist   = (E + ET + 255) / 256;
-    const int gb_wave_n = (N * 64 + 255) / 256;
-    const int pairs_s   = b2 ? N : (rows_s + 1) / 2;
-    const int pairs_t   = (N + 1) / 2;
-    const int bs_blocks = (pairs_s * 4 + 255) / 256;
-    const int bt_blocks = (pairs_t * 4 + 255) / 256;
-    const int gb_fuse   = (rows_s * 4 + 255) / 256;
+    const int nlb    = (N + 63) / 64;
+
+    const int gb_init  = (tot_s + 255) / 256;
+    const int gb_castt = ((int)nd + 255) / 256;
+    const int gb_hist  = (E + ET + 255) / 256;
 
     hipMemsetAsync(cnt_s, 0, (size_t)N * 4, stream);
     hipMemsetAsync(cnt_t, 0, (size_t)N * 4, stream);
@@ -641,35 +700,45 @@
     k_fill_all<<<gb_hist, 256, 0, stream>>>(src, dst, edge_type, off_s, cnt_s, pk_s,
                                             tsrc, tdst, off_t, cnt_t, pk_t, E, ET);
 
-    k_init_onehot<<<gb_init, 256, 0, stream>>>(
-        x_s, (unsigned*)xbf_s, h_index, N, tot_s, b2);
-    k_cast_init<<<gb_castt, 256, 0, stream>>>(rel_text_init, x_t, xbf_t, (int)nd);
+    k_init_onehot<<<gb_init, 256, 0, stream>>>(x_s, mirA_s, h_index, N, tot_s, b2);
+    k_cast_init<<<gb_castt, 256, 0, stream>>>(rel_text_init, x_t, mirA_t, (int)nd);
 
     for (int i = 0; i < L; ++i) {
+        const unsigned* mis = (i & 1) ? mirB_s : mirA_s;
+        unsigned*       mos = (i & 1) ? mirA_s : mirB_s;
+        const unsigned short* mit = (i & 1) ? mirB_t : mirA_t;
+        unsigned short*       mot = (i & 1) ? mirA_t : mirB_t;
         if (b2) {
-            k_gather_all<<<2 * gb_wave_n, 256, 0, stream>>>(
-                (const unsigned*)xbf_s, agg_s, off_s, pk_s,
+            k_layer_all<<<2 * nlb, 256, 0, stream>>>(
+                mis, mos, x_s, off_s, pk_s,
                 struct_rel + (size_t)i * R * 64, h_index,
-                xbf_t, agg_t, off_t, pk_t, text_rel + (size_t)i * 64, rel_text_init,
-                N, gb_wave_n, gb_wave_n);
+                struct_W + (size_t)i * 128 * 64, struct_b + i * 64,
+                struct_g + i * 64, struct_beta + i * 64,
+                mit, mot, x_t, off_t, pk_t,
+                text_rel + (size_t)i * 64, rel_text_init,
+                text_W + (size_t)i * 128 * 64, text_b + i * 64,
+                text_g + i * 64, text_beta + i * 64,
+                N, nlb, nlb);
         } else {
             k_gather_struct_gen<<<(rows_s * 64 + 255) / 256, 256, 0, stream>>>(
-                x_s, agg_s, off_s, pk_s,
+                x_s, agg_gen, off_s, pk_s,
                 struct_rel + (size_t)i * R * 64, h_index, N, rows_s);
-            k_gather_all<<<gb_wave_n, 256, 0, stream>>>(
-                (const unsigned*)xbf_s, agg_s, off_s, pk_s,
+            k_update_gen<<<(rows_s * 4 + 255) / 256, 256, 0, stream>>>(
+                struct_W + (size_t)i * 128 * 64, struct_b + i * 64,
+                struct_g + i * 64, struct_beta + i * 64, x_s, agg_gen, rows_s);
+            k_layer_all<<<nlb, 256, 0, stream>>>(
+                nullptr, nullptr, x_s, off_s, pk_s,
                 struct_rel + (size_t)i * R * 64, h_index,
-                xbf_t, agg_t, off_t, pk_t, text_rel + (size_t)i * 64, rel_text_init,
-                N, 0, gb_wave_n);
-        }
-        k_update_all<<<bs_blocks + bt_blocks, 256, 0, stream>>>(
-            struct_W + (size_t)i * 128 * 64, struct_b + i * 64,
-            struct_g + i * 64, struct_beta + i * 64, x_s, xbf_s, agg_s, rows_s,
-            text_W + (size_t)i * 128 * 64, text_b + i * 64,
-            text_g + i * 64, text_beta + i * 64, x_t, xbf_t, agg_t, N,
-            bs_blocks, bt_blocks, N, b2);
-    }
-
-    k_fuse<<<gb_fuse, 256, 0, stream>>>(
+                struct_W + (size_t)i * 128 * 64, struct_b + i * 64,
+                struct_g + i * 64, struct_beta + i * 64,
+                mit, mot, x_t, off_t, pk_t,
+                text_rel + (size_t)i * 64, rel_text_init,
+                text_W + (size_t)i * 128 * 64, text_b + i * 64,
+                text_g + i * 64, text_beta + i * 64,
+                N, 0, nlb);
+        }
+    }
+
+    k_fuse<<<(rows_s * 4 + 255) / 256, 256, 0, stream>>>(
         fuse_W1, fuse_b1, fuse_W2, fuse_b2, x_s, x_t, N, rows_s);
 }
```
